# Optimization experiments

Measured on AMD Instinct MI355X. Metric: run time of the kernel, lower is better.

## Reference

```python
import jax, jax.numpy as jnp
import numpy as np

IN_DIM = 2048
OUT_DIM = 2048
BATCH = 4096

def _xavier(key, fan_in, fan_out):
    std = np.sqrt(2.0 / (fan_in + fan_out)).astype(np.float32)
    return jax.random.normal(key, (fan_in, fan_out), dtype=jnp.float32) * std

def setup_inputs() -> dict:
    key = jax.random.key(0)
    ks = jax.random.split(key, 12)
    inp = {
        'X': jax.random.normal(ks[0], (BATCH, IN_DIM), dtype=jnp.float32),
        'C': jax.random.normal(ks[1], (BATCH, OUT_DIM), dtype=jnp.float32),
        'H': jax.random.normal(ks[2], (BATCH, OUT_DIM), dtype=jnp.float32),
        'W_xf': _xavier(ks[3], IN_DIM, OUT_DIM),
        'W_xg': _xavier(ks[4], IN_DIM, OUT_DIM),
        'W_xi': _xavier(ks[5], IN_DIM, OUT_DIM),
        'W_xo': _xavier(ks[6], IN_DIM, OUT_DIM),
        'W_hf': _xavier(ks[7], OUT_DIM, OUT_DIM),
        'W_hg': _xavier(ks[8], OUT_DIM, OUT_DIM),
        'W_hi': _xavier(ks[9], OUT_DIM, OUT_DIM),
        'W_ho': _xavier(ks[10], OUT_DIM, OUT_DIM),
        'b_f': jnp.zeros((1, OUT_DIM), dtype=jnp.float32),
        'b_g': jnp.zeros((1, OUT_DIM), dtype=jnp.float32),
        'b_i': jnp.zeros((1, OUT_DIM), dtype=jnp.float32),
        'b_o': jnp.zeros((1, OUT_DIM), dtype=jnp.float32),
    }
    return inp

def reference(X, C, H, W_xf, W_xg, W_xi, W_xo, W_hf, W_hg, W_hi, W_ho, b_f, b_g, b_i, b_o):
    # LSTM cell: 4 gates, each x@W_x* + b_* + h@W_h*
    F = jax.nn.sigmoid(X @ W_xf + b_f + H @ W_hf)
    I = jax.nn.sigmoid(X @ W_xi + b_i + H @ W_hi)
    O = jax.nn.sigmoid(X @ W_xo + b_o + H @ W_ho)
    G = jnp.tanh(X @ W_xg + b_g + H @ W_hg)
    C_new = G * I + F * C
    Y = O * jnp.tanh(C_new)
    return (C_new, Y)
```

## Files before the change

### kernel.cpp

```cpp
#include <hip/hip_runtime.h>
#include <cstdint>
#include <cstddef>

#define BATCH   4096
#define IN_DIM  2048
#define OUT_DIM 2048
#define KDIM    4096
#define NT      128

typedef __bf16 bf16x8 __attribute__((ext_vector_type(8)));
typedef float  floatx4 __attribute__((ext_vector_type(4)));

__device__ __forceinline__ unsigned short f2bf(float f) {
  unsigned int u = __float_as_uint(f);
  u += 0x7FFFu + ((u >> 16) & 1u);
  return (unsigned short)(u >> 16);
}

__device__ __forceinline__ void async16(const void* g, void* l) {
  __builtin_amdgcn_global_load_lds(
      (const __attribute__((address_space(1))) unsigned int*)g,
      (__attribute__((address_space(3))) unsigned int*)l, 16, 0, 0);
}

__device__ __forceinline__ float tanh_fast(float x) {
  return 1.f - 2.f / (__expf(2.f * x) + 1.f);
}

__global__ __launch_bounds__(256) void pack_A_kernel(
    const float* __restrict__ X, const float* __restrict__ H,
    unsigned short* __restrict__ A) {
  int idx = blockIdx.x * 256 + threadIdx.x;
  int e = idx << 2;
  int m = e >> 12;
  int k = e & 4095;
  const float* src = (k < IN_DIM) ? (X + (size_t)m * IN_DIM + k)
                                  : (H + (size_t)m * OUT_DIM + (k - IN_DIM));
  float4 v = *(const float4*)src;
  ushort4 o;
  o.x = f2bf(v.x); o.y = f2bf(v.y); o.z = f2bf(v.z); o.w = f2bf(v.w);
  *(ushort4*)(A + e) = o;
}

__global__ __launch_bounds__(256) void pack_B_kernel(
    const float* __restrict__ Wxf, const float* __restrict__ Wxi,
    const float* __restrict__ Wxo, const float* __restrict__ Wxg,
    const float* __restrict__ Whf, const float* __restrict__ Whi,
    const float* __restrict__ Who, const float* __restrict__ Whg,
    unsigned short* __restrict__ Bt) {
  __shared__ float tile[64][33];
  int bx = blockIdx.x;
  int kT = bx & 63;
  int nT = bx >> 6;
  int k0 = kT * 64, n0 = nT * 32;
  int g = n0 >> 11;
  int c0 = n0 & 2047;
  const float* W;
  int kk0;
  if (k0 < IN_DIM) {
    kk0 = k0;
    W = (g == 0) ? Wxf : (g == 1) ? Wxi : (g == 2) ? Wxo : Wxg;
  } else {
    kk0 = k0 - IN_DIM;
    W = (g == 0) ? Whf : (g == 1) ? Whi : (g == 2) ? Who : Whg;
  }
  int t = threadIdx.x;
#pragma unroll
  for (int i = 0; i < 2; ++i) {
    int idx = i * 256 + t;
    int lk = idx >> 3, lc = (idx & 7) * 4;
    float4 v = *(const float4*)(W + (size_t)(kk0 + lk) * 2048 + c0 + lc);
    tile[lk][lc]     = v.x;
    tile[lk][lc + 1] = v.y;
    tile[lk][lc + 2] = v.z;
    tile[lk][lc + 3] = v.w;
  }
  __syncthreads();
  int ln = t >> 3, k8 = (t & 7) * 8;
  unsigned int p[4];
#pragma unroll
  for (int j = 0; j < 4; ++j) {
    unsigned int lo = f2bf(tile[k8 + 2 * j][ln]);
    unsigned int hi = f2bf(tile[k8 + 2 * j + 1][ln]);
    p[j] = lo | (hi << 16);
  }
  uint4 o = make_uint4(p[0], p[1], p[2], p[3]);
  *(uint4*)(Bt + (size_t)(n0 + ln) * KDIM + k0 + k8) = o;
}

template <bool LAST, bool IG1, bool IG2>
__device__ __forceinline__ void do_tile(
    const char* sl, char* sn,
    const char* aG_1, const char* aG_2, const char* bG_1, const char* bG_2,
    unsigned kbG1, unsigned kbG2, int t16,
    int aOffA, int bOff, floatx4 (&acc)[4][8]) {
  bf16x8 af[4], bfr[4];
  if (LAST) asm volatile("s_waitcnt vmcnt(1)" ::: "memory");
  else      asm volatile("s_waitcnt vmcnt(4)" ::: "memory");
  asm volatile("s_barrier" ::: "memory");
#pragma unroll
  for (int mt = 0; mt < 4; ++mt)
    af[mt] = *(const bf16x8*)(sl + aOffA + mt * 1024);
#pragma unroll
  for (int nf = 0; nf < 4; ++nf)
    bfr[nf] = *(const bf16x8*)(sl + bOff + nf * 4096);
  if (IG2) async16(aG_2 + kbG2, sn + 8192 + t16);
  __builtin_amdgcn_s_setprio(1);
#pragma unroll
  for (int nf = 0; nf < 4; ++nf)
#pragma unroll
    for (int mt = 0; mt < 4; ++mt)
      acc[nf][mt] = __builtin_amdgcn_mfma_f32_16x16x32_bf16(
          af[mt], bfr[nf], acc[nf][mt], 0, 0, 0);
  __builtin_amdgcn_s_setprio(0);
  if (LAST) asm volatile("s_waitcnt vmcnt(0)" ::: "memory");
  else      asm volatile("s_waitcnt vmcnt(4)" ::: "memory");
  asm volatile("s_barrier" ::: "memory");
#pragma unroll
  for (int mt = 0; mt < 4; ++mt)
    af[mt] = *(const bf16x8*)(sl + aOffA + 8192 + mt * 1024);
  if (IG1) {
    char* sc = const_cast<char*>(sl);
    async16(aG_1 + kbG1, sc + t16);
    async16(bG_1 + kbG1, sc + 16384 + t16);
    async16(bG_2 + kbG1, sc + 24576 + t16);
  }
  __builtin_amdgcn_s_setprio(1);
#pragma unroll
  for (int nf = 0; nf < 4; ++nf)
#pragma unroll
    for (int mt = 0; mt < 4; ++mt)
      acc[nf][mt + 4] = __builtin_amdgcn_mfma_f32_16x16x32_bf16(
          af[mt], bfr[nf], acc[nf][mt + 4], 0, 0, 0);
  __builtin_amdgcn_s_setprio(0);
}

__global__ __launch_bounds__(512, 2) void lstm_gemm_fused(
    const unsigned short* __restrict__ A,
    const unsigned short* __restrict__ Bt,
    const float* __restrict__ Cin,
    const float* __restrict__ bF, const float* __restrict__ bI,
    const float* __restrict__ bO, const float* __restrict__ bG,
    float* __restrict__ outC, float* __restrict__ outY) {
  __shared__ __align__(16) char smem[65536];

  const int t = threadIdx.x;
  const int lane = t & 63;
  const int w = t >> 6;
  const int wm = w >> 2;
  const int wn = w & 3;

  const int orig = blockIdx.x;
  const int wgid = (orig & 7) * 64 + (orig >> 3);
  const int bx = wgid & 31;
  const int by = wgid >> 5;
  const int mBase = by * 256;

  floatx4 acc[4][8];
#pragma unroll
  for (int g = 0; g < 4; ++g)
#pragma unroll
    for (int mt = 0; mt < 8; ++mt) acc[g][mt] = (floatx4){0.f, 0.f, 0.f, 0.f};

  const int rowT = t >> 2;
  const int cswz = ((t & 3) ^ ((t >> 3) & 3)) * 16;
  const int physA = rowT + (rowT & 64);
  const char* aG_1 = (const char*)A + ((size_t)(mBase + physA) * KDIM) * 2 + cswz;
  const char* aG_2 = aG_1 + (size_t)64 * KDIM * 2;
  const int bRow = (rowT >> 6) * 2048 + bx * 64 + (rowT & 63);
  const char* bG_1 = (const char*)Bt + ((size_t)bRow * KDIM) * 2 + cswz;
  const char* bG_2 = bG_1 + (size_t)4096 * KDIM * 2;
  const int t16 = t * 16;

  const int fr = lane & 15;
  const int fkxB = (((lane >> 4) ^ ((fr >> 1) & 3))) * 16;
  const int aOffA = (wm * 64 + fr) * 64 + fkxB;
  const int bOff = 16384 + (wn * 16 + fr) * 64 + fkxB;

  async16(aG_1,      smem + t16);
  async16(bG_1,      smem + 16384 + t16);
  async16(bG_2,      smem + 24576 + t16);
  async16(aG_2,      smem + 8192 + t16);
  async16(aG_1 + 64, smem + 32768 + t16);
  async16(bG_1 + 64, smem + 32768 + 16384 + t16);
  async16(bG_2 + 64, smem + 32768 + 24576 + t16);

  for (int tt = 0; tt < NT - 2; ++tt) {
    const char* sl = smem + (tt & 1) * 32768;
    char* sn = smem + ((tt + 1) & 1) * 32768;
    do_tile<false, true, true>(sl, sn, aG_1, aG_2, bG_1, bG_2,
                               (unsigned)(tt + 2) * 64, (unsigned)(tt + 1) * 64,
                               t16, aOffA, bOff, acc);
  }
  {
    const int tt = NT - 2;
    const char* sl = smem + (tt & 1) * 32768;
    char* sn = smem + ((tt + 1) & 1) * 32768;
    do_tile<false, false, true>(sl, sn, aG_1, aG_2, bG_1, bG_2,
                                0, (unsigned)(tt + 1) * 64,
                                t16, aOffA, bOff, acc);
  }
  {
    const int tt = NT - 1;
    const char* sl = smem + (tt & 1) * 32768;
    char* sn = smem + ((tt + 1) & 1) * 32768;
    do_tile<true, false, false>(sl, sn, aG_1, aG_2, bG_1, bG_2,
                                0, 0, t16, aOffA, bOff, acc);
  }

  const int col = bx * 64 + wn * 16 + fr;
  const float bfv = bF[col], biv = bI[col], bov = bO[col], bgv = bG[col];
  const int rb = mBase + wm * 128 + ((lane >> 4) << 2);
#pragma unroll
  for (int mt = 0; mt < 8; ++mt) {
#pragma unroll
    for (int r = 0; r < 4; ++r) {
      const int row = rb + mt * 16 + r;
      const size_t off = (size_t)row * OUT_DIM + col;
      float pf = acc[0][mt][r] + bfv;
      float pi = acc[1][mt][r] + biv;
      float po = acc[2][mt][r] + bov;
      float pg = acc[3][mt][r] + bgv;
      float F = 1.f / (1.f + __expf(-pf));
      float I = 1.f / (1.f + __expf(-pi));
      float O = 1.f / (1.f + __expf(-po));
      float G = tanh_fast(pg);
      float c_new = G * I + F * Cin[off];
      outC[off] = c_new;
      outY[off] = O * tanh_fast(c_new);
    }
  }
}

extern "C" void kernel_launch(void* const* d_in, const int* in_sizes, int n_in,
                              void* d_out, int out_size, void* d_ws, size_t ws_size,
                              hipStream_t stream) {
  const float* X   = (const float*)d_in[0];
  const float* C   = (const float*)d_in[1];
  const float* H   = (const float*)d_in[2];
  const float* Wxf = (const float*)d_in[3];
  const float* Wxg = (const float*)d_in[4];
  const float* Wxi = (const float*)d_in[5];
  const float* Wxo = (const float*)d_in[6];
  const float* Whf = (const float*)d_in[7];
  const float* Whg = (const float*)d_in[8];
  const float* Whi = (const float*)d_in[9];
  const float* Who = (const float*)d_in[10];
  const float* bf_ = (const float*)d_in[11];
  const float* bg_ = (const float*)d_in[12];
  const float* bi_ = (const float*)d_in[13];
  const float* bo_ = (const float*)d_in[14];

  float* outC = (float*)d_out;
  float* outY = (float*)d_out + (size_t)BATCH * OUT_DIM;

  unsigned short* A  = (unsigned short*)d_ws;
  unsigned short* Bt = A + (size_t)BATCH * KDIM;

  pack_A_kernel<<<(BATCH * KDIM / 4) / 256, 256, 0, stream>>>(X, H, A);
  pack_B_kernel<<<64 * 256, 256, 0, stream>>>(Wxf, Wxi, Wxo, Wxg,
                                              Whf, Whi, Who, Whg, Bt);
  lstm_gemm_fused<<<dim3(512), dim3(512), 0, stream>>>(
      A, Bt, C, bf_, bi_, bo_, bg_, outC, outY);
}
```

Baseline: 525.8 us.

## Shrink GEMM block tile to 128x256 with 4 waves and 1024 blocks

The fused LSTM GEMM goes from 512-thread blocks covering 256 rows by 4 gates x 64 columns to 256-thread blocks covering 128 rows. Each wave now handles 64 rows by 32 columns per gate, and the gate halves are split across two MFMA phases by B fragment instead of by A rows. The shared-memory double buffer shrinks to 48 KB, and the load schedule and vmcnt waits are reworked to match. Smaller tiles double the block count and may improve occupancy and latency hiding, but they lower arithmetic intensity, since each A tile is reused over fewer columns, so more global/L2 traffic is needed.

```diff
diff --git a/kernel.cpp b/kernel.cpp
--- a/kernel.cpp
+++ b/kernel.cpp
@@ -90,144 +90,170 @@
 
 template <bool LAST, bool IG1, bool IG2>
 __device__ __forceinline__ void do_tile(
-    const char* sl, char* sn,
-    const char* aG_1, const char* aG_2, const char* bG_1, const char* bG_2,
+    const char* sl, char* snA, char* snB,
+    const char* aG1, const char* aG2, const char* bGp0, const char* bGp1,
+    const char* bGp2, const char* bGp3,
     unsigned kbG1, unsigned kbG2, int t16,
-    int aOffA, int bOff, floatx4 (&acc)[4][8]) {
-  bf16x8 af[4], bfr[4];
-  if (LAST) asm volatile("s_waitcnt vmcnt(1)" ::: "memory");
-  else      asm volatile("s_waitcnt vmcnt(4)" ::: "memory");
+    int aOff, int bOff, floatx4 (&acc)[4][2][4]) {
+  bf16x8 af[4], bfr[2][2];
+  if (LAST) asm volatile("s_waitcnt vmcnt(2)" ::: "memory");
+  else      asm volatile("s_waitcnt vmcnt(6)" ::: "memory");
   asm volatile("s_barrier" ::: "memory");
 #pragma unroll
   for (int mt = 0; mt < 4; ++mt)
-    af[mt] = *(const bf16x8*)(sl + aOffA + mt * 1024);
-#pragma unroll
-  for (int nf = 0; nf < 4; ++nf)
-    bfr[nf] = *(const bf16x8*)(sl + bOff + nf * 4096);
-  if (IG2) async16(aG_2 + kbG2, sn + 8192 + t16);
+    af[mt] = *(const bf16x8*)(sl + aOff + mt * 1024);
+#pragma unroll
+  for (int g = 0; g < 2; ++g)
+#pragma unroll
+    for (int nf2 = 0; nf2 < 2; ++nf2)
+      bfr[g][nf2] = *(const bf16x8*)(sl + bOff + g * 4096 + nf2 * 1024);
+  if (IG2) {
+    async16(bGp2 + kbG2, snB + 16384 + t16);
+    async16(bGp3 + kbG2, snB + 20480 + t16);
+  }
   __builtin_amdgcn_s_setprio(1);
 #pragma unroll
-  for (int nf = 0; nf < 4; ++nf)
-#pragma unroll
-    for (int mt = 0; mt < 4; ++mt)
-      acc[nf][mt] = __builtin_amdgcn_mfma_f32_16x16x32_bf16(
-          af[mt], bfr[nf], acc[nf][mt], 0, 0, 0);
+  for (int g = 0; g < 2; ++g)
+#pragma unroll
+    for (int nf2 = 0; nf2 < 2; ++nf2)
+#pragma unroll
+      for (int mt = 0; mt < 4; ++mt)
+        acc[g][nf2][mt] = __builtin_amdgcn_mfma_f32_16x16x32_bf16(
+            af[mt], bfr[g][nf2], acc[g][nf2][mt], 0, 0, 0);
   __builtin_amdgcn_s_setprio(0);
   if (LAST) asm volatile("s_waitcnt vmcnt(0)" ::: "memory");
-  else      asm volatile("s_waitcnt vmcnt(4)" ::: "memory");
+  else      asm volatile("s_waitcnt vmcnt(6)" ::: "memory");
   asm volatile("s_barrier" ::: "memory");
 #pragma unroll
-  for (int mt = 0; mt < 4; ++mt)
-    af[mt] = *(const bf16x8*)(sl + aOffA + 8192 + mt * 1024);
+  for (int g = 0; g < 2; ++g)
+#pragma unroll
+    for (int nf2 = 0; nf2 < 2; ++nf2)
+      bfr[g][nf2] = *(const bf16x8*)(sl + bOff + (g + 2) * 4096 + nf2 * 1024);
   if (IG1) {
-    char* sc = const_cast<char*>(sl);
-    async16(aG_1 + kbG1, sc + t16);
-    async16(bG_1 + kbG1, sc + 16384 + t16);
-    async16(bG_2 + kbG1, sc + 24576 + t16);
+    async16(aG1 + kbG1, snA + t16);
+    async16(aG2 + kbG1, snA + 4096 + t16);
+    async16(bGp0 + kbG1, snA + 8192 + t16);
+    async16(bGp1 + kbG1, snA + 12288 + t16);
   }
   __builtin_amdgcn_s_setprio(1);
 #pragma unroll
-  for (int nf = 0; nf < 4; ++nf)
-#pragma unroll
-    for (int mt = 0; mt < 4; ++mt)
-      acc[nf][mt + 4] = __builtin_amdgcn_mfma_f32_16x16x32_bf16(
-          af[mt], bfr[nf], acc[nf][mt + 4], 0, 0, 0);
+  for (int g = 0; g < 2; ++g)
+#pragma unroll
+    for (int nf2 = 0; nf2 < 2; ++nf2)
+#pragma unroll
+      for (int mt = 0; mt < 4; ++mt)
+        acc[g + 2][nf2][mt] = __builtin_amdgcn_mfma_f32_16x16x32_bf16(
+            af[mt], bfr[g][nf2], acc[g + 2][nf2][mt], 0, 0, 0);
   __builtin_amdgcn_s_setprio(0);
 }
 
-__global__ __launch_bounds__(512, 2) void lstm_gemm_fused(
+__global__ __launch_bounds__(256, 2) void lstm_gemm_fused(
     const unsigned short* __restrict__ A,
     const unsigned short* __restrict__ Bt,
     const float* __restrict__ Cin,
     const float* __restrict__ bF, const float* __restrict__ bI,
     const float* __restrict__ bO, const float* __restrict__ bG,
     float* __restrict__ outC, float* __restrict__ outY) {
-  __shared__ __align__(16) char smem[65536];
+  __shared__ __align__(16) char smem[49152];
 
   const int t = threadIdx.x;
   const int lane = t & 63;
   const int w = t >> 6;
-  const int wm = w >> 2;
-  const int wn = w & 3;
+  const int wm = w >> 1;
+  const int wn = w & 1;
 
   const int orig = blockIdx.x;
-  const int wgid = (orig & 7) * 64 + (orig >> 3);
+  const int wgid = (orig & 7) * 128 + (orig >> 3);
   const int bx = wgid & 31;
   const int by = wgid >> 5;
-  const int mBase = by * 256;
-
-  floatx4 acc[4][8];
+  const int mBase = by * 128;
+
+  floatx4 acc[4][2][4];
 #pragma unroll
   for (int g = 0; g < 4; ++g)
 #pragma unroll
-    for (int mt = 0; mt < 8; ++mt) acc[g][mt] = (floatx4){0.f, 0.f, 0.f, 0.f};
+    for (int nf2 = 0; nf2 < 2; ++nf2)
+#pragma unroll
+      for (int mt = 0; mt < 4; ++mt)
+        acc[g][nf2][mt] = (floatx4){0.f, 0.f, 0.f, 0.f};
 
   const int rowT = t >> 2;
   const int cswz = ((t & 3) ^ ((t >> 3) & 3)) * 16;
-  const int physA = rowT + (rowT & 64);
-  const char* aG_1 = (const char*)A + ((size_t)(mBase + physA) * KDIM) * 2 + cswz;
-  const char* aG_2 = aG_1 + (size_t)64 * KDIM * 2;
-  const int bRow = (rowT >> 6) * 2048 + bx * 64 + (rowT & 63);
-  const char* bG_1 = (const char*)Bt + ((size_t)bRow * KDIM) * 2 + cswz;
-  const char* bG_2 = bG_1 + (size_t)4096 * KDIM * 2;
+  const char* aG1 = (const char*)A + ((size_t)(mBase + rowT) * KDIM) * 2 + cswz;
+  const char* aG2 = aG1 + (size_t)64 * KDIM * 2;
+  const char* bGp0 = (const char*)Bt +
+      ((size_t)(0 * 2048 + bx * 64 + rowT) * KDIM) * 2 + cswz;
+  const char* bGp1 = bGp0 + (size_t)2048 * KDIM * 2;
+  const char* bGp2 = bGp0 + (size_t)4096 * KDIM * 2;
+  const char* bGp3 = bGp0 + (size_t)6144 * KDIM * 2;
   const int t16 = t * 16;
 
   const int fr = lane & 15;
   const int fkxB = (((lane >> 4) ^ ((fr >> 1) & 3))) * 16;
-  const int aOffA = (wm * 64 + fr) * 64 + fkxB;
-  const int bOff = 16384 + (wn * 16 + fr) * 64 + fkxB;
-
-  async16(aG_1,      smem + t16);
-  async16(bG_1,      smem + 16384 + t16);
-  async16(bG_2,      smem + 24576 + t16);
-  async16(aG_2,      smem + 8192 + t16);
-  async16(aG_1 + 64, smem + 32768 + t16);
-  async16(bG_1 + 64, smem + 32768 + 16384 + t16);
-  async16(bG_2 + 64, smem + 32768 + 24576 + t16);
+  const int aOff = (wm * 64 + fr) * 64 + fkxB;
+  const int bOff = 8192 + (wn * 32 + fr) * 64 + fkxB;
+
+  async16(aG1,       smem + t16);
+  async16(aG2,       smem + 4096 + t16);
+  async16(bGp0,      smem + 8192 + t16);
+  async16(bGp1,      smem + 12288 + t16);
+  async16(bGp2,      smem + 16384 + t16);
+  async16(bGp3,      smem + 20480 + t16);
+  async16(aG1 + 64,  smem + 24576 + t16);
+  async16(aG2 + 64,  smem + 24576 + 4096 + t16);
+  async16(bGp0 + 64, smem + 24576 + 8192 + t16);
+  async16(bGp1 + 64, smem + 24576 + 12288 + t16);
 
   for (int tt = 0; tt < NT - 2; ++tt) {
-    const char* sl = smem + (tt & 1) * 32768;
-    char* sn = smem + ((tt + 1) & 1) * 32768;
-    do_tile<false, true, true>(sl, sn, aG_1, aG_2, bG_1, bG_2,
+    const char* sl = smem + (tt & 1) * 24576;
+    char* snA = const_cast<char*>(sl);
+    char* snB = smem + ((tt + 1) & 1) * 24576;
+    do_tile<false, true, true>(sl, snA, snB, aG1, aG2, bGp0, bGp1, bGp2, bGp3,
                                (unsigned)(tt + 2) * 64, (unsigned)(tt + 1) * 64,
-                               t16, aOffA, bOff, acc);
+                               t16, aOff, bOff, acc);
   }
   {
     const int tt = NT - 2;
-    const char* sl = smem + (tt & 1) * 32768;
-    char* sn = smem + ((tt + 1) & 1) * 32768;
-    do_tile<false, false, true>(sl, sn, aG_1, aG_2, bG_1, bG_2,
+    const char* sl = smem + (tt & 1) * 24576;
+    char* snA = const_cast<char*>(sl);
+    char* snB = smem + ((tt + 1) & 1) * 24576;
+    do_tile<false, false, true>(sl, snA, snB, aG1, aG2, bGp0, bGp1, bGp2, bGp3,
                                 0, (unsigned)(tt + 1) * 64,
-                                t16, aOffA, bOff, acc);
+                                t16, aOff, bOff, acc);
   }
   {
     const int tt = NT - 1;
-    const char* sl = smem + (tt & 1) * 32768;
-    char* sn = smem + ((tt + 1) & 1) * 32768;
-    do_tile<true, false, false>(sl, sn, aG_1, aG_2, bG_1, bG_2,
-                                0, 0, t16, aOffA, bOff, acc);
-  }
-
-  const int col = bx * 64 + wn * 16 + fr;
-  const float bfv = bF[col], biv = bI[col], bov = bO[col], bgv = bG[col];
-  const int rb = mBase + wm * 128 + ((lane >> 4) << 2);
-#pragma unroll
-  for (int mt = 0; mt < 8; ++mt) {
-#pragma unroll
-    for (int r = 0; r < 4; ++r) {
-      const int row = rb + mt * 16 + r;
-      const size_t off = (size_t)row * OUT_DIM + col;
-      float pf = acc[0][mt][r] + bfv;
-      float pi = acc[1][mt][r] + biv;
-      float po = acc[2][mt][r] + bov;
-      float pg = acc[3][mt][r] + bgv;
-      float F = 1.f / (1.f + __expf(-pf));
-      float I = 1.f / (1.f + __expf(-pi));
-      float O = 1.f / (1.f + __expf(-po));
-      float G = tanh_fast(pg);
-      float c_new = G * I + F * Cin[off];
-      outC[off] = c_new;
-      outY[off] = O * tanh_fast(c_new);
+    const char* sl = smem + (tt & 1) * 24576;
+    char* snA = const_cast<char*>(sl);
+    char* snB = smem + ((tt + 1) & 1) * 24576;
+    do_tile<true, false, false>(sl, snA, snB, aG1, aG2, bGp0, bGp1, bGp2, bGp3,
+                                0, 0, t16, aOff, bOff, acc);
+  }
+
+  const int col0 = bx * 64 + wn * 32 + fr;
+  const int rb = mBase + wm * 64 + ((lane >> 4) << 2);
+#pragma unroll
+  for (int nf2 = 0; nf2 < 2; ++nf2) {
+    const int col = col0 + nf2 * 16;
+    const float bfv = bF[col], biv = bI[col], bov = bO[col], bgv = bG[col];
+#pragma unroll
+    for (int mt = 0; mt < 4; ++mt) {
+#pragma unroll
+      for (int r = 0; r < 4; ++r) {
+        const int row = rb + mt * 16 + r;
+        const size_t off = (size_t)row * OUT_DIM + col;
+        float pf = acc[0][nf2][mt][r] + bfv;
+        float pi = acc[1][nf2][mt][r] + biv;
+        float po = acc[2][nf2][mt][r] + bov;
+        float pg = acc[3][nf2][mt][r] + bgv;
+        float F = 1.f / (1.f + __expf(-pf));
+        float I = 1.f / (1.f + __expf(-pi));
+        float O = 1.f / (1.f + __expf(-po));
+        float G = tanh_fast(pg);
+        float c_new = G * I + F * Cin[off];
+        outC[off] = c_new;
+        outY[off] = O * tanh_fast(c_new);
+      }
     }
   }
 }
@@ -260,6 +286,6 @@
   pack_A_kernel<<<(BATCH * KDIM / 4) / 256, 256, 0, stream>>>(X, H, A);
   pack_B_kernel<<<64 * 256, 256, 0, stream>>>(Wxf, Wxi, Wxo, Wxg,
                                               Whf, Whi, Who, Whg, Bt);
-  lstm_gemm_fused<<<dim3(512), dim3(512), 0, stream>>>(
+  lstm_gemm_fused<<<dim3(1024), dim3(256), 0, stream>>>(
       A, Bt, C, bf_, bi_, bo_, bg_, outC, outY);
 }
```

Result: slower. 619.5 us (+17.8%).

## Widen weight-pack tiles and remap GEMM workgroups into 8x8 L2-friendly blocks

Applied to the files above, without the earlier changes.

The weight transpose/pack kernel now handles 64x128 tiles per block instead of 64x32, with each thread writing four 16-byte chunks. This cuts the block count and makes writes to the transposed buffer longer and contiguous. The GEMM workgroup-to-tile mapping changes from a simple XCD-strided order to 8x8 super-tiles per XCD group, aiming to improve L2 reuse of A and B panels. The wait-count helper is a cosmetic refactor. The larger shared tile may lower pack-kernel occupancy.

```diff
diff --git a/kernel.cpp b/kernel.cpp
--- a/kernel.cpp
+++ b/kernel.cpp
@@ -21,6 +21,13 @@
   __builtin_amdgcn_global_load_lds(
       (const __attribute__((address_space(1))) unsigned int*)g,
       (__attribute__((address_space(3))) unsigned int*)l, 16, 0, 0);
+}
+
+template <int N>
+__device__ __forceinline__ void waitv() {
+  if constexpr (N == 0)      asm volatile("s_waitcnt vmcnt(0)" ::: "memory");
+  else if constexpr (N == 1) asm volatile("s_waitcnt vmcnt(1)" ::: "memory");
+  else if constexpr (N == 4) asm volatile("s_waitcnt vmcnt(4)" ::: "memory");
 }
 
 __device__ __forceinline__ float tanh_fast(float x) {
@@ -48,13 +55,13 @@
     const float* __restrict__ Whf, const float* __restrict__ Whi,
     const float* __restrict__ Who, const float* __restrict__ Whg,
     unsigned short* __restrict__ Bt) {
-  __shared__ float tile[64][33];
-  int bx = blockIdx.x;
-  int kT = bx & 63;
-  int nT = bx >> 6;
-  int k0 = kT * 64, n0 = nT * 32;
-  int g = n0 >> 11;
-  int c0 = n0 & 2047;
+  __shared__ float tile[64][129];
+  int bid = blockIdx.x;
+  int kT = bid & 63;
+  int nT = bid >> 6;
+  int k0 = kT * 64;
+  int g  = nT >> 4;
+  int c0 = (nT & 15) * 128;
   const float* W;
   int kk0;
   if (k0 < IN_DIM) {
@@ -66,9 +73,10 @@
   }
   int t = threadIdx.x;
 #pragma unroll
-  for (int i = 0; i < 2; ++i) {
+  for (int i = 0; i < 8; ++i) {
     int idx = i * 256 + t;
-    int lk = idx >> 3, lc = (idx & 7) * 4;
+    int lk = idx >> 5;
+    int lc = (idx & 31) * 4;
     float4 v = *(const float4*)(W + (size_t)(kk0 + lk) * 2048 + c0 + lc);
     tile[lk][lc]     = v.x;
     tile[lk][lc + 1] = v.y;
@@ -76,16 +84,22 @@
     tile[lk][lc + 3] = v.w;
   }
   __syncthreads();
-  int ln = t >> 3, k8 = (t & 7) * 8;
-  unsigned int p[4];
-#pragma unroll
-  for (int j = 0; j < 4; ++j) {
-    unsigned int lo = f2bf(tile[k8 + 2 * j][ln]);
-    unsigned int hi = f2bf(tile[k8 + 2 * j + 1][ln]);
-    p[j] = lo | (hi << 16);
-  }
-  uint4 o = make_uint4(p[0], p[1], p[2], p[3]);
-  *(uint4*)(Bt + (size_t)(n0 + ln) * KDIM + k0 + k8) = o;
+  int ln = t >> 1;
+  int half = t & 1;
+  const size_t nrow = (size_t)(g * 2048 + c0 + ln);
+  uint4* dst = (uint4*)(Bt + nrow * KDIM + k0) + half * 4;
+#pragma unroll
+  for (int jj = 0; jj < 4; ++jj) {
+    int j = half * 4 + jj;
+    unsigned int p[4];
+#pragma unroll
+    for (int q = 0; q < 4; ++q) {
+      unsigned int lo = f2bf(tile[j * 8 + 2 * q][ln]);
+      unsigned int hi = f2bf(tile[j * 8 + 2 * q + 1][ln]);
+      p[q] = lo | (hi << 16);
+    }
+    dst[jj] = make_uint4(p[0], p[1], p[2], p[3]);
+  }
 }
 
 template <bool LAST, bool IG1, bool IG2>
@@ -95,8 +109,7 @@
     unsigned kbG1, unsigned kbG2, int t16,
     int aOffA, int bOff, floatx4 (&acc)[4][8]) {
   bf16x8 af[4], bfr[4];
-  if (LAST) asm volatile("s_waitcnt vmcnt(1)" ::: "memory");
-  else      asm volatile("s_waitcnt vmcnt(4)" ::: "memory");
+  if (LAST) waitv<1>(); else waitv<4>();
   asm volatile("s_barrier" ::: "memory");
 #pragma unroll
   for (int mt = 0; mt < 4; ++mt)
@@ -113,8 +126,7 @@
       acc[nf][mt] = __builtin_amdgcn_mfma_f32_16x16x32_bf16(
           af[mt], bfr[nf], acc[nf][mt], 0, 0, 0);
   __builtin_amdgcn_s_setprio(0);
-  if (LAST) asm volatile("s_waitcnt vmcnt(0)" ::: "memory");
-  else      asm volatile("s_waitcnt vmcnt(4)" ::: "memory");
+  if (LAST) waitv<0>(); else waitv<4>();
   asm volatile("s_barrier" ::: "memory");
 #pragma unroll
   for (int mt = 0; mt < 4; ++mt)
@@ -151,9 +163,10 @@
   const int wn = w & 3;
 
   const int orig = blockIdx.x;
-  const int wgid = (orig & 7) * 64 + (orig >> 3);
-  const int bx = wgid & 31;
-  const int by = wgid >> 5;
+  const int x = orig & 7;
+  const int u = orig >> 3;
+  const int bx = (x & 3) * 8 + (u & 7);
+  const int by = (x >> 2) * 8 + (u >> 3);
   const int mBase = by * 256;
 
   floatx4 acc[4][8];
@@ -189,7 +202,8 @@
     const char* sl = smem + (tt & 1) * 32768;
     char* sn = smem + ((tt + 1) & 1) * 32768;
     do_tile<false, true, true>(sl, sn, aG_1, aG_2, bG_1, bG_2,
-                               (unsigned)(tt + 2) * 64, (unsigned)(tt + 1) * 64,
+                               (unsigned)(tt + 2) * 64,
+                               (unsigned)(tt + 1) * 64,
                                t16, aOffA, bOff, acc);
   }
   {
@@ -258,8 +272,8 @@
   unsigned short* Bt = A + (size_t)BATCH * KDIM;
 
   pack_A_kernel<<<(BATCH * KDIM / 4) / 256, 256, 0, stream>>>(X, H, A);
-  pack_B_kernel<<<64 * 256, 256, 0, stream>>>(Wxf, Wxi, Wxo, Wxg,
-                                              Whf, Whi, Who, Whg, Bt);
+  pack_B_kernel<<<4096, 256, 0, stream>>>(Wxf, Wxi, Wxo, Wxg,
+                                          Whf, Whi, Who, Whg, Bt);
   lstm_gemm_fused<<<dim3(512), dim3(512), 0, stream>>>(
       A, Bt, C, bf_, bi_, bo_, bg_, outC, outY);
 }
```

Result: faster. 496.1 us (-5.6%).
